# Optimization experiments

Measured on AMD Instinct MI355X. Metric: run time of the kernel, lower is better.

Reference implementation:

```python
import jax, jax.numpy as jnp
import numpy as np

B, S, D, H = 4, 2048, 1024, 16
HD = D // H  # head_dim = 64


def setup_inputs() -> dict:
    key = jax.random.key(0)
    ks = jax.random.split(key, 14)
    s = 0.02
    return {
        "inputs_q": jax.random.normal(ks[0], (B, S, D), jnp.float32),
        "pos_emb_q": jax.random.normal(ks[1], (1, S, D), jnp.float32),
        "pos_emb_k": jax.random.normal(ks[2], (1, S, D), jnp.float32),
        "pos_emb_v": jax.random.normal(ks[3], (1, S, D), jnp.float32),
        "attention_bias": jax.random.normal(ks[4], (1, 1, S, S), jnp.float32),
        "attention_bias_kv": jax.random.normal(ks[5], (B, S), jnp.float32),
        "wq": jax.random.normal(ks[6], (D, H, HD), jnp.float32) * s,
        "bq": jnp.zeros((H, HD), jnp.float32),
        "wk": jax.random.normal(ks[7], (D, H, HD), jnp.float32) * s,
        "bk": jnp.zeros((H, HD), jnp.float32),
        "wv": jax.random.normal(ks[8], (D, H, HD), jnp.float32) * s,
        "bv": jnp.zeros((H, HD), jnp.float32),
        "wo": jax.random.normal(ks[9], (H, HD, D), jnp.float32) * s,
        "bo": jnp.zeros((D,), jnp.float32),
    }


def reference(inputs_q, pos_emb_q, pos_emb_k, pos_emb_v, attention_bias,
              attention_bias_kv, wq, bq, wk, bk, wv, bv, wo, bo):
    # Self-attention: inputs_kv = inputs_q. Additive pos-embs BEFORE projection.
    q_in = inputs_q + pos_emb_q
    k_in = inputs_q + pos_emb_k
    v_in = inputs_q + pos_emb_v
    # QKV DenseGeneral: [B,S,D] -> [B,S,H,HD]
    q = jnp.einsum('bsd,dhk->bshk', q_in, wq) + bq
    k = jnp.einsum('bsd,dhk->bshk', k_in, wk) + bk
    v = jnp.einsum('bsd,dhk->bshk', v_in, wv) + bv
    # Scaled dot-product attention with full bias + key-only bias.
    q = q / jnp.sqrt(jnp.asarray(HD, q.dtype))
    scores = jnp.einsum('bqhk,bshk->bhqs', q, k)  # [B,H,Sq,Sk]
    scores = scores + attention_bias + attention_bias_kv[:, None, None, :]
    attn = jax.nn.softmax(scores, axis=-1)
    x = jnp.einsum('bhqs,bshk->bqhk', attn, v)  # [B,S,H,HD]
    # Output projection contracting (H, HD) -> D.
    out = jnp.einsum('bqhk,hkd->bqd', x, wo) + bo
    return out
```

## Files before the change

### kernel.cpp

```cpp
#include <hip/hip_runtime.h>

typedef __attribute__((ext_vector_type(8))) short short8;
typedef __attribute__((ext_vector_type(4))) float f32x4;

#define MFMA16(a, b, c) __builtin_amdgcn_mfma_f32_16x16x32_bf16(a, b, c, 0, 0, 0)

#define SEQ 2048
#define DIM 1024
#define NH 16
#define HD 64
#define LOG2E 1.4426950408889634f

__device__ __forceinline__ ushort f2bf(float f) {
  union { float f; unsigned u; } v; v.f = f;
  unsigned r = (v.u + 0x7FFFu + ((v.u >> 16) & 1u)) >> 16;
  return (ushort)r;
}

__device__ __forceinline__ ushort bf1(float f) {
  unsigned r;
  asm("v_cvt_pk_bf16_f32 %0, %1, %2" : "=v"(r) : "v"(f), "v"(f));
  return (ushort)(r & 0xffffu);
}

__device__ __forceinline__ float exp2fn(float x) {
#if __has_builtin(__builtin_amdgcn_exp2f)
  return __builtin_amdgcn_exp2f(x);
#else
  return exp2f(x);
#endif
}

__global__ __launch_bounds__(256) void prep_a(
    const float* __restrict__ x, const float* __restrict__ pq,
    const float* __restrict__ pk, const float* __restrict__ pv,
    ushort* __restrict__ aq, ushort* __restrict__ ak, ushort* __restrict__ av) {
  int i = (blockIdx.x * 256 + threadIdx.x) * 4;
  int pi = i & (SEQ * DIM - 1);
  float4 xv = *(const float4*)(x + i);
  float4 q4 = *(const float4*)(pq + pi);
  float4 k4 = *(const float4*)(pk + pi);
  float4 v4 = *(const float4*)(pv + pi);
  ushort4 o;
  o.x = f2bf(xv.x + q4.x); o.y = f2bf(xv.y + q4.y);
  o.z = f2bf(xv.z + q4.z); o.w = f2bf(xv.w + q4.w);
  *(ushort4*)(aq + i) = o;
  o.x = f2bf(xv.x + k4.x); o.y = f2bf(xv.y + k4.y);
  o.z = f2bf(xv.z + k4.z); o.w = f2bf(xv.w + k4.w);
  *(ushort4*)(ak + i) = o;
  o.x = f2bf(xv.x + v4.x); o.y = f2bf(xv.y + v4.y);
  o.z = f2bf(xv.z + v4.z); o.w = f2bf(xv.w + v4.w);
  *(ushort4*)(av + i) = o;
}

__global__ __launch_bounds__(256) void transpose_all(
    const float* __restrict__ w0, const float* __restrict__ w1,
    const float* __restrict__ w2, const float* __restrict__ w3,
    ushort* __restrict__ d0, ushort* __restrict__ d1,
    ushort* __restrict__ d2, ushort* __restrict__ d3) {
  const int z = blockIdx.z;
  const float* src = z == 0 ? w0 : z == 1 ? w1 : z == 2 ? w2 : w3;
  ushort* dst = z == 0 ? d0 : z == 1 ? d1 : z == 2 ? d2 : d3;
  __shared__ float t[32][33];
  int tx = threadIdx.x & 31, ty = threadIdx.x >> 5;
  int x0 = blockIdx.x * 32, y0 = blockIdx.y * 32;
#pragma unroll
  for (int j = 0; j < 32; j += 8) t[ty + j][tx] = src[(size_t)(y0 + ty + j) * DIM + x0 + tx];
  __syncthreads();
#pragma unroll
  for (int j = 0; j < 32; j += 8)
    dst[(size_t)(x0 + ty + j) * DIM + y0 + tx] = f2bf(t[tx][ty + j]);
}

__global__ __launch_bounds__(256) void gemm_qkv(
    const ushort* __restrict__ aq, const ushort* __restrict__ ak,
    const ushort* __restrict__ av, const ushort* __restrict__ wqT,
    const ushort* __restrict__ wkT, const ushort* __restrict__ wvT,
    const float* __restrict__ bq, const float* __restrict__ bk,
    const float* __restrict__ bv, ushort* __restrict__ Qb,
    ushort* __restrict__ Kb, ushort* __restrict__ VTb) {
  constexpr int K = 1024, LDA = 40;
  __shared__ __align__(16) ushort As[128 * LDA];
  __shared__ __align__(16) ushort Bs[128 * LDA];
  const int proj = blockIdx.y >> 3, bn = blockIdx.y & 7, bm = blockIdx.x;
  const ushort* A = proj == 0 ? aq : proj == 1 ? ak : av;
  const ushort* Bt = proj == 0 ? wqT : proj == 1 ? wkT : wvT;
  const float* bias = proj == 0 ? bq : proj == 1 ? bk : bv;
  ushort* outp = proj == 0 ? Qb : proj == 1 ? Kb : VTb;
  const float scale = proj == 0 ? 0.125f * LOG2E : 1.0f;

  const int tid = threadIdx.x;
  const int wave = tid >> 6, lane = tid & 63;
  const int wr = wave >> 1, wc = wave & 1;
  const int g = lane >> 4, l15 = lane & 15;
  const int r0 = tid >> 2, c0 = (tid & 3) * 8;
  const ushort* Ap = A + (size_t)(bm * 128 + r0) * K + c0;
  const ushort* Bp = Bt + (size_t)(bn * 128 + r0) * K + c0;
  f32x4 acc[4][4] = {};

  uint4 ra0 = *(const uint4*)(Ap);
  uint4 ra1 = *(const uint4*)(Ap + (size_t)64 * K);
  uint4 rb0 = *(const uint4*)(Bp);
  uint4 rb1 = *(const uint4*)(Bp + (size_t)64 * K);

  for (int kt = 0; kt < K; kt += 32) {
    __syncthreads();
    *(uint4*)&As[r0 * LDA + c0] = ra0;
    *(uint4*)&As[(r0 + 64) * LDA + c0] = ra1;
    *(uint4*)&Bs[r0 * LDA + c0] = rb0;
    *(uint4*)&Bs[(r0 + 64) * LDA + c0] = rb1;
    __syncthreads();
    if (kt + 32 < K) {
      ra0 = *(const uint4*)(Ap + kt + 32);
      ra1 = *(const uint4*)(Ap + (size_t)64 * K + kt + 32);
      rb0 = *(const uint4*)(Bp + kt + 32);
      rb1 = *(const uint4*)(Bp + (size_t)64 * K + kt + 32);
    }
    short8 af[4], bfr[4];
#pragma unroll
    for (int m = 0; m < 4; ++m)
      af[m] = *(const short8*)&As[(wr * 64 + m * 16 + l15) * LDA + g * 8];
#pragma unroll
    for (int n = 0; n < 4; ++n)
      bfr[n] = *(const short8*)&Bs[(wc * 64 + n * 16 + l15) * LDA + g * 8];
#pragma unroll
    for (int m = 0; m < 4; ++m)
#pragma unroll
      for (int n = 0; n < 4; ++n) acc[m][n] = MFMA16(af[m], bfr[n], acc[m][n]);
  }

#pragma unroll
  for (int m = 0; m < 4; ++m) {
    int row = bm * 128 + wr * 64 + m * 16 + g * 4;
#pragma unroll
    for (int n = 0; n < 4; ++n) {
      int col = bn * 128 + wc * 64 + n * 16 + l15;
      float bv2 = bias[col];
#pragma unroll
      for (int j = 0; j < 4; ++j) {
        float v = (acc[m][n][j] + bv2) * scale;
        int r = row + j;
        int b = r >> 11, s = r & (SEQ - 1), h = col >> 6, hd = col & (HD - 1);
        if (proj < 2)
          outp[((size_t)((b * NH + h) * SEQ + s)) * HD + hd] = f2bf(v);
        else
          outp[((size_t)((b * NH + h) * HD + hd)) * SEQ + s] = f2bf(v);
      }
    }
  }
}

__global__ __launch_bounds__(256) void gemm_out(
    const ushort* __restrict__ A, const ushort* __restrict__ Bt,
    const float* __restrict__ bias, float* __restrict__ outp) {
  constexpr int K = 1024, LDA = 40;
  __shared__ __align__(16) ushort As[128 * LDA];
  __shared__ __align__(16) ushort Bs[128 * LDA];
  const int tid = threadIdx.x;
  const int wave = tid >> 6, lane = tid & 63;
  const int wr = wave >> 1, wc = wave & 1;
  const int g = lane >> 4, l15 = lane & 15;
  const int bm = blockIdx.x, bn = blockIdx.y;
  const int r0 = tid >> 2, c0 = (tid & 3) * 8;
  const ushort* Ap = A + (size_t)(bm * 128 + r0) * K + c0;
  const ushort* Bp = Bt + (size_t)(bn * 128 + r0) * K + c0;
  f32x4 acc[4][4] = {};

  uint4 ra0 = *(const uint4*)(Ap);
  uint4 ra1 = *(const uint4*)(Ap + (size_t)64 * K);
  uint4 rb0 = *(const uint4*)(Bp);
  uint4 rb1 = *(const uint4*)(Bp + (size_t)64 * K);

  for (int kt = 0; kt < K; kt += 32) {
    __syncthreads();
    *(uint4*)&As[r0 * LDA + c0] = ra0;
    *(uint4*)&As[(r0 + 64) * LDA + c0] = ra1;
    *(uint4*)&Bs[r0 * LDA + c0] = rb0;
    *(uint4*)&Bs[(r0 + 64) * LDA + c0] = rb1;
    __syncthreads();
    if (kt + 32 < K) {
      ra0 = *(const uint4*)(Ap + kt + 32);
      ra1 = *(const uint4*)(Ap + (size_t)64 * K + kt + 32);
      rb0 = *(const uint4*)(Bp + kt + 32);
      rb1 = *(const uint4*)(Bp + (size_t)64 * K + kt + 32);
    }
    short8 af[4], bfr[4];
#pragma unroll
    for (int m = 0; m < 4; ++m)
      af[m] = *(const short8*)&As[(wr * 64 + m * 16 + l15) * LDA + g * 8];
#pragma unroll
    for (int n = 0; n < 4; ++n)
      bfr[n] = *(const short8*)&Bs[(wc * 64 + n * 16 + l15) * LDA + g * 8];
#pragma unroll
    for (int m = 0; m < 4; ++m)
#pragma unroll
      for (int n = 0; n < 4; ++n) acc[m][n] = MFMA16(af[m], bfr[n], acc[m][n]);
  }

#pragma unroll
  for (int m = 0; m < 4; ++m) {
    int row = bm * 128 + wr * 64 + m * 16 + g * 4;
#pragma unroll
    for (int n = 0; n < 4; ++n) {
      int col = bn * 128 + wc * 64 + n * 16 + l15;
      float bv = bias[col];
#pragma unroll
      for (int j = 0; j < 4; ++j)
        outp[(size_t)(row + j) * DIM + col] = acc[m][n][j] + bv;
    }
  }
}

__global__ __launch_bounds__(256) void attn9(
    const ushort* __restrict__ Q, const ushort* __restrict__ K,
    const ushort* __restrict__ VT, const float* __restrict__ abias,
    const float* __restrict__ kvbias, ushort* __restrict__ X) {
  constexpr int LDK = 72, LDV = 72, LDP = 72;
  __shared__ __align__(16) ushort Ks[64 * LDK];
  __shared__ __align__(16) ushort Vs[64 * LDV];
  __shared__ __align__(16) ushort Ps[4][32 * LDP];
  const int tid = threadIdx.x;
  const int w = tid >> 6, lane = tid & 63, g = lane >> 4, l15 = lane & 15;
  const int px = blockIdx.x;
  const int qt = (px & 7) | ((px >> 9) << 3);
  const int bh = (px >> 3) & 63;
  const int b = bh >> 4, h = bh & (NH - 1);
  const int q0 = qt * 128;

  short8 qf[2][2];
#pragma unroll
  for (int sub = 0; sub < 2; ++sub) {
    const ushort* qp = Q + ((size_t)bh * SEQ + q0 + w * 32 + sub * 16 + l15) * HD;
#pragma unroll
    for (int c = 0; c < 2; ++c) qf[sub][c] = *(const short8*)(qp + c * 32 + g * 8);
  }

  f32x4 o[2][4] = {};
  float l_lane[2][4] = {};

  const int sr = tid >> 2, scc = (tid & 3) * 16;
  const ushort* Kp = K + (size_t)bh * SEQ * HD;
  const ushort* Vp = VT + (size_t)bh * HD * SEQ;
  const float* abp = abias + (size_t)q0 * SEQ;
  const float* kvp = kvbias + b * SEQ;

  uint4 ka = *(const uint4*)(Kp + (size_t)sr * HD + scc);
  uint4 kb = *(const uint4*)(Kp + (size_t)sr * HD + scc + 8);
  uint4 va = *(const uint4*)(Vp + (size_t)sr * SEQ + scc);
  uint4 vb = *(const uint4*)(Vp + (size_t)sr * SEQ + scc + 8);

  for (int kt = 0; kt < SEQ / 64; ++kt) {
    const int k0 = kt * 64;

    float bkv[4];
#pragma unroll
    for (int ct = 0; ct < 4; ++ct) bkv[ct] = kvp[k0 + ct * 16 + l15];
    float abf[2][4][4];
#pragma unroll
    for (int sub = 0; sub < 2; ++sub)
#pragma unroll
      for (int j = 0; j < 4; ++j) {
        const float* abr = abp + (size_t)(w * 32 + sub * 16 + 4 * g + j) * SEQ + k0 + l15;
#pragma unroll
        for (int ct = 0; ct < 4; ++ct) abf[sub][ct][j] = abr[ct * 16];
      }

    __syncthreads();
    *(uint4*)&Ks[sr * LDK + scc] = ka;
    *(uint4*)&Ks[sr * LDK + scc + 8] = kb;
    *(uint4*)&Vs[sr * LDV + scc] = va;
    *(uint4*)&Vs[sr * LDV + scc + 8] = vb;
    __syncthreads();

    if (kt + 1 < SEQ / 64) {
      ka = *(const uint4*)(Kp + (size_t)(k0 + 64 + sr) * HD + scc);
      kb = *(const uint4*)(Kp + (size_t)(k0 + 64 + sr) * HD + scc + 8);
      va = *(const uint4*)(Vp + (size_t)sr * SEQ + k0 + 64 + scc);
      vb = *(const uint4*)(Vp + (size_t)sr * SEQ + k0 + 64 + scc + 8);
    }

    f32x4 s4[2][4];
#pragma unroll
    for (int ct = 0; ct < 4; ++ct) {
      short8 kf0 = *(const short8*)&Ks[(ct * 16 + l15) * LDK + g * 8];
      short8 kf1 = *(const short8*)&Ks[(ct * 16 + l15) * LDK + 32 + g * 8];
#pragma unroll
      for (int sub = 0; sub < 2; ++sub) {
        f32x4 z = {0.f, 0.f, 0.f, 0.f};
        f32x4 t = MFMA16(qf[sub][0], kf0, z);
        s4[sub][ct] = MFMA16(qf[sub][1], kf1, t);
      }
    }

#pragma unroll
    for (int sub = 0; sub < 2; ++sub) {
      float p[4][4];
#pragma unroll
      for (int ct = 0; ct < 4; ++ct)
#pragma unroll
        for (int j = 0; j < 4; ++j)
          p[ct][j] = exp2fn(fmaf(abf[sub][ct][j] + bkv[ct], LOG2E, s4[sub][ct][j]));
#pragma unroll
      for (int j = 0; j < 4; ++j)
        l_lane[sub][j] += (p[0][j] + p[1][j]) + (p[2][j] + p[3][j]);
#pragma unroll
      for (int ct = 0; ct < 4; ++ct)
#pragma unroll
        for (int j = 0; j < 4; ++j)
          Ps[w][(sub * 16 + 4 * g + j) * LDP + ct * 16 + l15] = bf1(p[ct][j]);
    }

    asm volatile("s_waitcnt lgkmcnt(0)" ::: "memory");
    __builtin_amdgcn_sched_barrier(0);

    short8 pa[2][2];
#pragma unroll
    for (int sub = 0; sub < 2; ++sub)
#pragma unroll
      for (int ks = 0; ks < 2; ++ks)
        pa[sub][ks] = *(const short8*)&Ps[w][(sub * 16 + l15) * LDP + ks * 32 + g * 8];
#pragma unroll
    for (int ctd = 0; ctd < 4; ++ctd) {
      short8 vf0 = *(const short8*)&Vs[(ctd * 16 + l15) * LDV + g * 8];
      short8 vf1 = *(const short8*)&Vs[(ctd * 16 + l15) * LDV + 32 + g * 8];
#pragma unroll
      for (int sub = 0; sub < 2; ++sub) {
        o[sub][ctd] = MFMA16(pa[sub][0], vf0, o[sub][ctd]);
        o[sub][ctd] = MFMA16(pa[sub][1], vf1, o[sub][ctd]);
      }
    }
  }

#pragma unroll
  for (int sub = 0; sub < 2; ++sub) {
    float inv[4];
#pragma unroll
    for (int j = 0; j < 4; ++j) {
      float l = l_lane[sub][j];
      l += __shfl_xor(l, 1);
      l += __shfl_xor(l, 2);
      l += __shfl_xor(l, 4);
      l += __shfl_xor(l, 8);
      inv[j] = 1.0f / l;
    }
#pragma unroll
    for (int ctd = 0; ctd < 4; ++ctd)
#pragma unroll
      for (int j = 0; j < 4; ++j) {
        size_t row = (size_t)b * SEQ + q0 + w * 32 + sub * 16 + 4 * g + j;
        X[row * DIM + h * HD + ctd * 16 + l15] = bf1(o[sub][ctd][j] * inv[j]);
      }
  }
}

extern "C" void kernel_launch(void* const* d_in, const int* in_sizes, int n_in,
                              void* d_out, int out_size, void* d_ws, size_t ws_size,
                              hipStream_t stream) {
  const float* inputs_q = (const float*)d_in[0];
  const float* pos_q = (const float*)d_in[1];
  const float* pos_k = (const float*)d_in[2];
  const float* pos_v = (const float*)d_in[3];
  const float* abias = (const float*)d_in[4];
  const float* kvbias = (const float*)d_in[5];
  const float* wq = (const float*)d_in[6];
  const float* bq = (const float*)d_in[7];
  const float* wk = (const float*)d_in[8];
  const float* bk = (const float*)d_in[9];
  const float* wv = (const float*)d_in[10];
  const float* bv = (const float*)d_in[11];
  const float* wo = (const float*)d_in[12];
  const float* bo = (const float*)d_in[13];

  char* ws = (char*)d_ws;
  const size_t MB = 1ull << 20;
  ushort* wqT = (ushort*)(ws + 0 * MB);
  ushort* wkT = (ushort*)(ws + 2 * MB);
  ushort* wvT = (ushort*)(ws + 4 * MB);
  ushort* woT = (ushort*)(ws + 6 * MB);
  ushort* aq = (ushort*)(ws + 8 * MB);
  ushort* ak = (ushort*)(ws + 24 * MB);
  ushort* av = (ushort*)(ws + 40 * MB);
  ushort* Qb = (ushort*)(ws + 56 * MB);
  ushort* Kb = (ushort*)(ws + 72 * MB);
  ushort* VTb = (ushort*)(ws + 88 * MB);
  ushort* Xb = (ushort*)(ws + 8 * MB);

  prep_a<<<8192, 256, 0, stream>>>(inputs_q, pos_q, pos_k, pos_v, aq, ak, av);
  transpose_all<<<dim3(32, 32, 4), 256, 0, stream>>>(wq, wk, wv, wo, wqT, wkT, wvT, woT);
  gemm_qkv<<<dim3(64, 24), 256, 0, stream>>>(aq, ak, av, wqT, wkT, wvT,
                                             bq, bk, bv, Qb, Kb, VTb);
  attn9<<<1024, 256, 0, stream>>>(Qb, Kb, VTb, abias, kvbias, Xb);
  gemm_out<<<dim3(64, 8), 256, 0, stream>>>(Xb, woT, bo, (float*)d_out);
}
```

Measured before the change: 292.5 us.

## Halve attention query tile to 64 rows and reorder grid for bias reuse

The attention kernel now processes 64 query rows per block (16 per wave) instead of 128, doubling the grid to 2048 blocks and cutting per-thread registers. The block index is remapped so consecutive blocks cover all 64 batch-heads for one query tile, letting them share the same attention_bias rows in cache. Bias loads are moved after the shared-memory barrier. The aim is more occupancy and better L2 reuse of the large fp32 bias. The cost is that each K/V tile is loaded from global memory twice as often.

```diff
diff --git a/kernel.cpp b/kernel.cpp
--- a/kernel.cpp
+++ b/kernel.cpp
@@ -211,32 +211,31 @@
   }
 }
 
-__global__ __launch_bounds__(256) void attn9(
+__global__ __launch_bounds__(256) void attn10(
     const ushort* __restrict__ Q, const ushort* __restrict__ K,
     const ushort* __restrict__ VT, const float* __restrict__ abias,
     const float* __restrict__ kvbias, ushort* __restrict__ X) {
   constexpr int LDK = 72, LDV = 72, LDP = 72;
   __shared__ __align__(16) ushort Ks[64 * LDK];
   __shared__ __align__(16) ushort Vs[64 * LDV];
-  __shared__ __align__(16) ushort Ps[4][32 * LDP];
+  __shared__ __align__(16) ushort Ps[4][16 * LDP];
   const int tid = threadIdx.x;
   const int w = tid >> 6, lane = tid & 63, g = lane >> 4, l15 = lane & 15;
   const int px = blockIdx.x;
-  const int qt = (px & 7) | ((px >> 9) << 3);
-  const int bh = (px >> 3) & 63;
+  const int bh = px & 63;
+  const int qt = px >> 6;
   const int b = bh >> 4, h = bh & (NH - 1);
-  const int q0 = qt * 128;
-
-  short8 qf[2][2];
-#pragma unroll
-  for (int sub = 0; sub < 2; ++sub) {
-    const ushort* qp = Q + ((size_t)bh * SEQ + q0 + w * 32 + sub * 16 + l15) * HD;
-#pragma unroll
-    for (int c = 0; c < 2; ++c) qf[sub][c] = *(const short8*)(qp + c * 32 + g * 8);
-  }
-
-  f32x4 o[2][4] = {};
-  float l_lane[2][4] = {};
+  const int q0 = qt * 64;
+
+  short8 qf[2];
+  {
+    const ushort* qp = Q + ((size_t)bh * SEQ + q0 + w * 16 + l15) * HD;
+#pragma unroll
+    for (int c = 0; c < 2; ++c) qf[c] = *(const short8*)(qp + c * 32 + g * 8);
+  }
+
+  f32x4 o[4] = {};
+  float l_lane[4] = {};
 
   const int sr = tid >> 2, scc = (tid & 3) * 16;
   const ushort* Kp = K + (size_t)bh * SEQ * HD;
@@ -251,26 +250,23 @@
 
   for (int kt = 0; kt < SEQ / 64; ++kt) {
     const int k0 = kt * 64;
-
-    float bkv[4];
-#pragma unroll
-    for (int ct = 0; ct < 4; ++ct) bkv[ct] = kvp[k0 + ct * 16 + l15];
-    float abf[2][4][4];
-#pragma unroll
-    for (int sub = 0; sub < 2; ++sub)
-#pragma unroll
-      for (int j = 0; j < 4; ++j) {
-        const float* abr = abp + (size_t)(w * 32 + sub * 16 + 4 * g + j) * SEQ + k0 + l15;
-#pragma unroll
-        for (int ct = 0; ct < 4; ++ct) abf[sub][ct][j] = abr[ct * 16];
-      }
-
     __syncthreads();
     *(uint4*)&Ks[sr * LDK + scc] = ka;
     *(uint4*)&Ks[sr * LDK + scc + 8] = kb;
     *(uint4*)&Vs[sr * LDV + scc] = va;
     *(uint4*)&Vs[sr * LDV + scc + 8] = vb;
     __syncthreads();
+
+    float bkv[4];
+#pragma unroll
+    for (int ct = 0; ct < 4; ++ct) bkv[ct] = kvp[k0 + ct * 16 + l15];
+    float abf[4][4];
+#pragma unroll
+    for (int j = 0; j < 4; ++j) {
+      const float* abr = abp + (size_t)(w * 16 + 4 * g + j) * SEQ + k0 + l15;
+#pragma unroll
+      for (int ct = 0; ct < 4; ++ct) abf[ct][j] = abr[ct * 16];
+    }
 
     if (kt + 1 < SEQ / 64) {
       ka = *(const uint4*)(Kp + (size_t)(k0 + 64 + sr) * HD + scc);
@@ -279,78 +275,66 @@
       vb = *(const uint4*)(Vp + (size_t)sr * SEQ + k0 + 64 + scc + 8);
     }
 
-    f32x4 s4[2][4];
+    f32x4 s4[4];
 #pragma unroll
     for (int ct = 0; ct < 4; ++ct) {
       short8 kf0 = *(const short8*)&Ks[(ct * 16 + l15) * LDK + g * 8];
       short8 kf1 = *(const short8*)&Ks[(ct * 16 + l15) * LDK + 32 + g * 8];
-#pragma unroll
-      for (int sub = 0; sub < 2; ++sub) {
-        f32x4 z = {0.f, 0.f, 0.f, 0.f};
-        f32x4 t = MFMA16(qf[sub][0], kf0, z);
-        s4[sub][ct] = MFMA16(qf[sub][1], kf1, t);
-      }
-    }
-
-#pragma unroll
-    for (int sub = 0; sub < 2; ++sub) {
+      f32x4 z = {0.f, 0.f, 0.f, 0.f};
+      f32x4 t = MFMA16(qf[0], kf0, z);
+      s4[ct] = MFMA16(qf[1], kf1, t);
+    }
+
+    {
       float p[4][4];
 #pragma unroll
       for (int ct = 0; ct < 4; ++ct)
 #pragma unroll
         for (int j = 0; j < 4; ++j)
-          p[ct][j] = exp2fn(fmaf(abf[sub][ct][j] + bkv[ct], LOG2E, s4[sub][ct][j]));
+          p[ct][j] = exp2fn(fmaf(abf[ct][j] + bkv[ct], LOG2E, s4[ct][j]));
 #pragma unroll
       for (int j = 0; j < 4; ++j)
-        l_lane[sub][j] += (p[0][j] + p[1][j]) + (p[2][j] + p[3][j]);
+        l_lane[j] += (p[0][j] + p[1][j]) + (p[2][j] + p[3][j]);
 #pragma unroll
       for (int ct = 0; ct < 4; ++ct)
 #pragma unroll
         for (int j = 0; j < 4; ++j)
-          Ps[w][(sub * 16 + 4 * g + j) * LDP + ct * 16 + l15] = bf1(p[ct][j]);
+          Ps[w][(4 * g + j) * LDP + ct * 16 + l15] = bf1(p[ct][j]);
     }
 
     asm volatile("s_waitcnt lgkmcnt(0)" ::: "memory");
     __builtin_amdgcn_sched_barrier(0);
 
-    short8 pa[2][2];
-#pragma unroll
-    for (int sub = 0; sub < 2; ++sub)
-#pragma unroll
-      for (int ks = 0; ks < 2; ++ks)
-        pa[sub][ks] = *(const short8*)&Ps[w][(sub * 16 + l15) * LDP + ks * 32 + g * 8];
+    short8 pa[2];
+#pragma unroll
+    for (int ks = 0; ks < 2; ++ks)
+      pa[ks] = *(const short8*)&Ps[w][l15 * LDP + ks * 32 + g * 8];
 #pragma unroll
     for (int ctd = 0; ctd < 4; ++ctd) {
       short8 vf0 = *(const short8*)&Vs[(ctd * 16 + l15) * LDV + g * 8];
       short8 vf1 = *(const short8*)&Vs[(ctd * 16 + l15) * LDV + 32 + g * 8];
-#pragma unroll
-      for (int sub = 0; sub < 2; ++sub) {
-        o[sub][ctd] = MFMA16(pa[sub][0], vf0, o[sub][ctd]);
-        o[sub][ctd] = MFMA16(pa[sub][1], vf1, o[sub][ctd]);
-      }
-    }
-  }
-
-#pragma unroll
-  for (int sub = 0; sub < 2; ++sub) {
-    float inv[4];
+      o[ctd] = MFMA16(pa[0], vf0, o[ctd]);
+      o[ctd] = MFMA16(pa[1], vf1, o[ctd]);
+    }
+  }
+
+  float inv[4];
+#pragma unroll
+  for (int j = 0; j < 4; ++j) {
+    float l = l_lane[j];
+    l += __shfl_xor(l, 1);
+    l += __shfl_xor(l, 2);
+    l += __shfl_xor(l, 4);
+    l += __shfl_xor(l, 8);
+    inv[j] = 1.0f / l;
+  }
+#pragma unroll
+  for (int ctd = 0; ctd < 4; ++ctd)
 #pragma unroll
     for (int j = 0; j < 4; ++j) {
-      float l = l_lane[sub][j];
-      l += __shfl_xor(l, 1);
-      l += __shfl_xor(l, 2);
-      l += __shfl_xor(l, 4);
-      l += __shfl_xor(l, 8);
-      inv[j] = 1.0f / l;
-    }
-#pragma unroll
-    for (int ctd = 0; ctd < 4; ++ctd)
-#pragma unroll
-      for (int j = 0; j < 4; ++j) {
-        size_t row = (size_t)b * SEQ + q0 + w * 32 + sub * 16 + 4 * g + j;
-        X[row * DIM + h * HD + ctd * 16 + l15] = bf1(o[sub][ctd][j] * inv[j]);
-      }
-  }
+      size_t row = (size_t)b * SEQ + q0 + w * 16 + 4 * g + j;
+      X[row * DIM + h * HD + ctd * 16 + l15] = bf1(o[ctd][j] * inv[j]);
+    }
 }
 
 extern "C" void kernel_launch(void* const* d_in, const int* in_sizes, int n_in,
@@ -389,6 +373,6 @@
   transpose_all<<<dim3(32, 32, 4), 256, 0, stream>>>(wq, wk, wv, wo, wqT, wkT, wvT, woT);
   gemm_qkv<<<dim3(64, 24), 256, 0, stream>>>(aq, ak, av, wqT, wkT, wvT,
                                              bq, bk, bv, Qb, Kb, VTb);
-  attn9<<<1024, 256, 0, stream>>>(Qb, Kb, VTb, abias, kvbias, Xb);
+  attn10<<<2048, 256, 0, stream>>>(Qb, Kb, VTb, abias, kvbias, Xb);
   gemm_out<<<dim3(64, 8), 256, 0, stream>>>(Xb, woT, bo, (float*)d_out);
 }
```

Result: no change. 290.0 us (-0.8%).
